# Optimization experiments

Hardware: AMD Instinct MI355X
Metric: run time of the kernel (lower is better)

## Reference

```python
import jax, jax.numpy as jnp
from jax import lax
import numpy as np

BATCH = 8
INPUT_LEN = 768
OUTPUT_LEN = 192
MULTISCALE = (1, 2, 4)
HIDDEN = 256          # HiPPO order N == spectral channels
MODES = 32            # min(32, min(output_len, input_len)//2)
NUM_FEAT = 64


def hippo_matrices(N, dt):
    """HiPPO-LegT continuous matrices, bilinear-discretized (scipy cont2discrete equiv)."""
    Q = np.arange(N, dtype=np.float64)
    R = (2 * Q + 1)[:, None]
    j, i = np.meshgrid(Q, Q)
    A = np.where(i < j, -1.0, (-1.0) ** (i - j + 1)) * R
    B = ((-1.0) ** Q[:, None]) * R  # [N,1]
    I = np.eye(N)
    ima = I - (dt / 2.0) * A
    Ad = np.linalg.solve(ima, I + (dt / 2.0) * A)
    Bd = np.linalg.solve(ima, B * dt).squeeze(-1)
    return Ad.astype(np.float32), Bd.astype(np.float32)


def legendre_eval_matrix(N, dt):
    """eval_matrix[t, n] = P_n(1 - 2*vals[t]), vals = arange(0,1,dt)."""
    vals = np.arange(0.0, 1.0, dt)
    x = 1.0 - 2.0 * vals
    P = np.zeros((N, len(vals)), dtype=np.float64)
    P[0] = 1.0
    if N > 1:
        P[1] = x
    for n in range(1, N - 1):
        P[n + 1] = ((2 * n + 1) * x * P[n] - n * P[n - 1]) / (n + 1)
    return P.T.astype(np.float32)  # [len(vals), N]


def setup_inputs() -> dict:
    key = jax.random.key(0)
    k1, k2, k3, k4 = jax.random.split(key, 4)
    scale = 1.0 / (HIDDEN * HIDDEN)
    return {
        "inputs": jax.random.normal(k1, (BATCH, INPUT_LEN, NUM_FEAT), jnp.float32),
        "spec_wr": scale * jax.random.uniform(k2, (3, HIDDEN, HIDDEN, MODES), jnp.float32),
        "spec_wi": scale * jax.random.uniform(k3, (3, HIDDEN, HIDDEN, MODES), jnp.float32),
        "mlp_w": 0.1 * jax.random.normal(k4, (1, 3), jnp.float32),
        "mlp_b": jnp.zeros((1,), jnp.float32),
    }


def _film_forward(inputs, spec_wr, spec_wi, mlp_w, mlp_b):
    B_, _, D = inputs.shape
    preds = []
    for idx, scale in enumerate(MULTISCALE):
        dt = 1.0 / OUTPUT_LEN / scale
        Ad_np, Bd_np = hippo_matrices(HIDDEN, dt)
        em_np = legendre_eval_matrix(HIDDEN, dt)[-OUTPUT_LEN:]  # [out_len, N]
        Ad = jnp.asarray(Ad_np)
        Bd = jnp.asarray(Bd_np)
        em = jnp.asarray(em_np)
        T = scale * OUTPUT_LEN
        # HiPPO recurrence: c_t = c_{t-1} @ A^T + f_t * B  (sequential scan over time)
        f = jnp.transpose(inputs[:, -T:], (1, 0, 2))  # [T, B, D]

        def step(c, f_t, Ad=Ad, Bd=Bd):
            c = c @ Ad.T + f_t[..., None] * Bd
            return c, c

        c0 = jnp.zeros((B_, D, HIDDEN), inputs.dtype)
        _, cs = lax.scan(step, c0, f)               # [T, B, D, N]
        x = jnp.transpose(cs, (1, 2, 3, 0))          # [B, D, N, T]
        # SpectralConv1d: rfft -> complex mixing on low modes -> irfft
        x_ft = jnp.fft.rfft(x)                       # [B, D, N, T//2+1]
        w = (spec_wr[idx] + 1j * spec_wi[idx]).astype(jnp.complex64)  # [N, N, modes]
        out_m = jnp.einsum('bjix,iox->bjox', x_ft[..., :MODES], w)    # [B, D, N, modes]
        nfreq = T // 2 + 1
        out_ft = jnp.concatenate(
            [out_m, jnp.zeros(out_m.shape[:-1] + (nfreq - MODES,), out_m.dtype)], axis=-1)
        x = jnp.fft.irfft(out_ft, n=T)               # [B, D, N, T]
        # input_len >= output_len -> pick time index output_len-1, then project with Legendre
        x_out = x[:, :, :, OUTPUT_LEN - 1]           # [B, D, N]
        preds.append(x_out @ em.T)                   # [B, D, out_len]
    pred = jnp.stack(preds, axis=-1)                 # [B, D, out_len, 3]
    pred = jnp.squeeze(pred @ mlp_w.T + mlp_b, -1)   # [B, D, out_len]
    return jnp.transpose(pred, (0, 2, 1))            # [B, out_len, D]


def reference(inputs, spec_wr, spec_wi, mlp_w, mlp_b):
    return _film_forward(inputs, spec_wr, spec_wi, mlp_w, mlp_b)
```

## Files before the change

### kernel.cpp

```cpp
#include <hip/hip_runtime.h>


#define OFF_MF64  0
#define OFF_YA    1572864
#define OFF_YB    3145728
#define OFF_Z     4718592
#define OFF_F     7864320
#define OFF_PIV   8650752
#define OFF_FLAG  8653824
#define OFF_AP0   10223616
#define OFF_AP1   11010048
#define OFF_BD    11796480
#define OFF_V     11800576
#define OFF_EM    14159872
#define OFF_P     14749696
#define OFF_K     16125952
#define OFF_U4    29298688
#define OFF_WT4   117440512
#define OFF_C32   167772160
#define OFF_SEG4  211812352

typedef _Float16 half8 __attribute__((ext_vector_type(8)));
typedef float f32x4 __attribute__((ext_vector_type(4)));

__device__ __forceinline__ double a_entry(int i, int j){
  double base = (i < j) ? -1.0 : (((i - j) & 1) ? 1.0 : -1.0);
  return base * (double)(2*i + 1);
}

__device__ __forceinline__ unsigned int dpp_umax(unsigned int x){
  unsigned int t;
  t = (unsigned int)__builtin_amdgcn_update_dpp((int)x, (int)x, 0x111, 0xF, 0xF, false); x = x > t ? x : t;
  t = (unsigned int)__builtin_amdgcn_update_dpp((int)x, (int)x, 0x112, 0xF, 0xF, false); x = x > t ? x : t;
  t = (unsigned int)__builtin_amdgcn_update_dpp((int)x, (int)x, 0x114, 0xF, 0xE, false); x = x > t ? x : t;
  t = (unsigned int)__builtin_amdgcn_update_dpp((int)x, (int)x, 0x118, 0xF, 0xC, false); x = x > t ? x : t;
  t = (unsigned int)__builtin_amdgcn_update_dpp((int)x, (int)x, 0x142, 0xA, 0xF, false); x = x > t ? x : t;
  t = (unsigned int)__builtin_amdgcn_update_dpp((int)x, (int)x, 0x143, 0xC, 0xF, false); x = x > t ? x : t;
  return x;
}

__global__ void k_init(double* __restrict__ Mf64, float* __restrict__ em,
                       int* __restrict__ flags){
  int s = blockIdx.y, i = blockIdx.x, j = threadIdx.x;
  if (i < 256){
    double dt = (1.0 / 192.0) / (double)(1 << s);
    double m = ((i == j) ? 1.0 : 0.0) - 0.5 * dt * a_entry(i, j);
    Mf64[((size_t)s*256 + i)*256 + j] = m;
  } else {
    if (j < 192){
      int T = 192 << s;
      double dt = (1.0 / 192.0) / (double)(1 << s);
      double x = 1.0 - 2.0 * ((double)(T - 192 + j) * dt);
      float* row = em + ((size_t)s*192 + j)*256;
      double p0 = 1.0, p1 = x;
      row[0] = 1.0f; row[1] = (float)x;
      for (int n = 1; n < 255; ++n){
        double p2 = ((double)(2*n+1) * x * p1 - (double)n * p0) / (double)(n+1);
        row[n+1] = (float)p2;
        p0 = p1; p1 = p2;
      }
    } else if (j < 200){
      flags[s*8 + (j - 192)] = 0;
    }
  }
}

__global__ __launch_bounds__(256) void k_gj(float* __restrict__ Fg,
                                            int* __restrict__ pivg,
                                            int* __restrict__ flags,
                                            double* __restrict__ Ya){
  int s = blockIdx.x >> 4;
  int g = blockIdx.x & 15;
  int r = threadIdx.x;
  int c0 = g*32;
  float row[32];
  if (g < 8){
    double dt = (1.0 / 192.0) / (double)(1 << s);
    #pragma unroll
    for (int j = 0; j < 32; ++j){
      int col = c0 + j;
      row[j] = (float)(((r == col) ? 1.0 : 0.0) - 0.5*dt*a_entry(r, col));
    }
  } else {
    #pragma unroll
    for (int j = 0; j < 32; ++j) row[j] = (r == c0 - 256 + j) ? 1.f : 0.f;
  }
  __shared__ float Fl[32*256];
  __shared__ float prow[2][32];
  __shared__ float prow1[32];
  __shared__ int pvs[32];
  __shared__ unsigned int wv[4];
  __shared__ int invp[256];
  int used = 0;
  int* flagS = flags + s*8;
  int nrep = (g < 8) ? g : 8;
  for (int kp = 0; kp < nrep; ++kp){
    if (r == 0){
      int cnt = 0;
      while (__hip_atomic_load(&flagS[kp], __ATOMIC_ACQUIRE, __HIP_MEMORY_SCOPE_AGENT) == 0){
        __builtin_amdgcn_s_sleep(8);
        if (++cnt > 100000000) break;
      }
    }
    __syncthreads();
    const float* Fp = Fg + ((size_t)(s*8 + kp))*8192;
    #pragma unroll
    for (int l = 0; l < 32; ++l) Fl[l*256 + r] = Fp[l*256 + r];
    if (r < 32) pvs[r] = pivg[s*256 + kp*32 + r];
    __syncthreads();
    #pragma unroll
    for (int l = 0; l < 32; ++l) if (pvs[l] == r) used = 1;
    for (int l = 0; l < 32; ++l){
      int piv = pvs[l];
      float fv = Fl[l*256 + r];
      if (r == piv){
        #pragma unroll
        for (int j = 0; j < 32; ++j){ row[j] *= fv; prow[l & 1][j] = row[j]; }
      }
      __syncthreads();
      if (r != piv){
        #pragma unroll
        for (int j = 0; j < 32; ++j) row[j] -= fv * prow[l & 1][j];
      }
    }
    __syncthreads();
  }
  if (g < 8){
    float freg[32];
    #pragma unroll
    for (int l = 0; l < 32; ++l){
      float av = fabsf(row[l]);
      unsigned int kb = __builtin_bit_cast(unsigned int, av);
      unsigned int key = used ? 0u : ((kb & 0xFFFFFF00u) | (unsigned int)(255 - r));
      key = dpp_umax(key);
      if ((r & 63) == 63) wv[r >> 6] = key;
      __syncthreads();
      unsigned int b0 = wv[0] > wv[1] ? wv[0] : wv[1];
      unsigned int b1 = wv[2] > wv[3] ? wv[2] : wv[3];
      unsigned int best = b0 > b1 ? b0 : b1;
      int piv = 255 - (int)(best & 0xFFu);
      if (r == piv){
        float inv = 1.0f / row[l];
        freg[l] = inv;
        used = 1;
        #pragma unroll
        for (int j = 0; j < 32; ++j){ row[j] *= inv; prow1[j] = row[j]; }
      }
      if (r == 0) pvs[l] = piv;
      __syncthreads();
      if (r != piv){
        float f = row[l];
        freg[l] = f;
        #pragma unroll
        for (int j = 0; j < 32; ++j) row[j] -= f * prow1[j];
      }
    }
    float* Fgp = Fg + ((size_t)(s*8 + g))*8192;
    #pragma unroll
    for (int l = 0; l < 32; ++l) Fgp[l*256 + r] = freg[l];
    if (r < 32) pivg[s*256 + g*32 + r] = pvs[r];
    __threadfence();
    __syncthreads();
    if (r == 0)
      __hip_atomic_store(&flagS[g], 1, __ATOMIC_RELEASE, __HIP_MEMORY_SCOPE_AGENT);
  } else {
    int p = pivg[s*256 + r];
    invp[p] = r;
    __syncthreads();
    int dst = invp[r];
    double* Yr = Ya + ((size_t)s*256 + dst)*256 + (c0 - 256);
    #pragma unroll
    for (int j = 0; j < 32; ++j) Yr[j] = (double)row[j];
  }
}

__global__ void k_mmZ(const double* __restrict__ M, const double* __restrict__ Y,
                      double* __restrict__ Z){
  int s = blockIdx.y;
  const double* A = M + (size_t)s*65536;
  const double* B = Y + (size_t)s*65536;
  int c = threadIdx.x, r0 = blockIdx.x * 8;
  double acc[8] = {0,0,0,0,0,0,0,0};
  for (int j = 0; j < 256; ++j){
    double b = B[(size_t)j*256 + c];
    #pragma unroll
    for (int q = 0; q < 8; ++q) acc[q] += A[(size_t)(r0+q)*256 + j] * b;
  }
  #pragma unroll
  for (int q = 0; q < 8; ++q) Z[(size_t)s*65536 + (size_t)(r0+q)*256 + c] = acc[q];
}

__global__ void k_mmN(const double* __restrict__ Y, const double* __restrict__ Z,
                      double* __restrict__ Yn){
  int s = blockIdx.y;
  const double* A = Y + (size_t)s*65536;
  const double* B = Z + (size_t)s*65536;
  int c = threadIdx.x, r0 = blockIdx.x * 8;
  double acc[8] = {0,0,0,0,0,0,0,0};
  for (int j = 0; j < 256; ++j){
    double b = B[(size_t)j*256 + c];
    #pragma unroll
    for (int q = 0; q < 8; ++q) acc[q] += A[(size_t)(r0+q)*256 + j] * b;
  }
  #pragma unroll
  for (int q = 0; q < 8; ++q)
    Yn[(size_t)s*65536 + (size_t)(r0+q)*256 + c] =
      2.0 * A[(size_t)(r0+q)*256 + c] - acc[q];
}

__global__ void k_final(const double* __restrict__ Y, float* __restrict__ Ad,
                        float* __restrict__ Bd, float* __restrict__ V){
  int s = blockIdx.y;
  const double* Ys = Y + (size_t)s*65536;
  if (blockIdx.x < 64){
    int c = threadIdx.x, r0 = blockIdx.x * 4;
    #pragma unroll
    for (int q = 0; q < 4; ++q){
      double v = 2.0 * Ys[(size_t)(r0+q)*256 + c] - ((r0+q) == c ? 1.0 : 0.0);
      Ad[(size_t)s*65536 + (size_t)(r0+q)*256 + c] = (float)v;
    }
  } else {
    int i = threadIdx.x;
    double dt = (1.0 / 192.0) / (double)(1 << s);
    double acc = 0.0;
    for (int j = 0; j < 256; ++j){
      double bj = dt * ((j & 1) ? -1.0 : 1.0) * (double)(2*j + 1);
      acc += Ys[(size_t)i*256 + j] * bj;
    }
    float b = (float)acc;
    Bd[s*256 + i] = b;
    V[((size_t)s*768 + 0)*256 + i] = b;
  }
}

__global__ void k_level(const float* __restrict__ Pin, float* __restrict__ Pout,
                        float* __restrict__ V, int L, int noSquare){
  int s = blockIdx.y;
  const float* A = Pin + (size_t)s*65536;
  int bx = blockIdx.x;
  if (bx < 64){
    if (noSquare) return;
    int c = threadIdx.x, r0 = bx * 4;
    float acc[4] = {0,0,0,0};
    for (int k = 0; k < 256; ++k){
      float b = A[(size_t)k*256 + c];
      #pragma unroll
      for (int q = 0; q < 4; ++q) acc[q] += A[(size_t)(r0+q)*256 + k] * b;
    }
    #pragma unroll
    for (int q = 0; q < 4; ++q) Pout[(size_t)s*65536 + (size_t)(r0+q)*256 + c] = acc[q];
  } else {
    int j = threadIdx.x;
    if (j >= L || L + j >= 768) return;
    int r0 = (bx - 64) * 4;
    float* Vs = V + (size_t)s*768*256;
    float acc[4] = {0,0,0,0};
    for (int k = 0; k < 256; ++k){
      float v = Vs[(size_t)j*256 + k];
      #pragma unroll
      for (int q = 0; q < 4; ++q) acc[q] += A[(size_t)(r0+q)*256 + k] * v;
    }
    #pragma unroll
    for (int q = 0; q < 4; ++q) Vs[(size_t)(L+j)*256 + r0 + q] = acc[q];
  }
}

__global__ void k_wt(const float* __restrict__ wr, const float* __restrict__ wi,
                     float* __restrict__ Wt4){
  int s = blockIdx.x, i = blockIdx.y, tid = threadIdx.x;
  size_t srcbase = ((size_t)s*256 + i)*256;
  float* dst = Wt4 + ((size_t)s*256 + i)*16384;
  for (int ph = 0; ph < 64; ++ph){
    int col = ph*256 + tid;
    int kl = col >> 9, ri = (col >> 8) & 1, o = col & 255;
    const float* src = ri ? wi : wr;
    dst[col] = src[(srcbase + o)*32 + kl];
  }
}

__device__ __forceinline__ void splitf16(float x, unsigned short &h, unsigned short &l){
  _Float16 hf = (_Float16)x;
  _Float16 lf = (_Float16)(x - (float)hf);
  h = __builtin_bit_cast(unsigned short, hf);
  l = __builtin_bit_cast(unsigned short, lf);
}
__device__ __forceinline__ unsigned int pk(unsigned short a, unsigned short b){
  return (unsigned int)a | ((unsigned int)b << 16);
}

__global__ __launch_bounds__(256) void k_ugemm(const float* __restrict__ V,
                                               const float* __restrict__ Wt4,
                                               float* __restrict__ U){
  int s = blockIdx.z;
  int Ts = 192 << s;
  int mt = blockIdx.y;
  if (mt*64 >= Ts) return;
  int nb = blockIdx.x * 64;
  const float* Vs = V + (size_t)s*768*256;
  const float* Bm = Wt4 + (size_t)s*256*16384;
  __shared__ unsigned int Ah[4*65*4], Al[4*65*4];
  __shared__ unsigned int Bh[4*65*4], Bl[4*65*4];
  int tid = threadIdx.x;
  int lane = tid & 63;
  int w = tid >> 6;
  int m0 = (w >> 1) * 32, n0 = (w & 1) * 32;
  int ml = lane & 15, quad = lane >> 4;
  f32x4 acc[2][2];
  #pragma unroll
  for (int t = 0; t < 2; ++t)
    #pragma unroll
    for (int u = 0; u < 2; ++u) acc[t][u] = (f32x4){0.f,0.f,0.f,0.f};

  int am = tid >> 2, akf = tid & 3;
  int bn = tid & 63, bq = tid >> 6;

  for (int kk = 0; kk < 8; ++kk){
    if (kk) __syncthreads();
    {
      const float* ap = &Vs[(size_t)(mt*64 + am)*256 + kk*32 + akf*8];
      float4 a0 = *(const float4*)ap;
      float4 a1 = *(const float4*)(ap + 4);
      unsigned short h[8], l[8];
      splitf16(a0.x*16.f, h[0], l[0]); splitf16(a0.y*16.f, h[1], l[1]);
      splitf16(a0.z*16.f, h[2], l[2]); splitf16(a0.w*16.f, h[3], l[3]);
      splitf16(a1.x*16.f, h[4], l[4]); splitf16(a1.y*16.f, h[5], l[5]);
      splitf16(a1.z*16.f, h[6], l[6]); splitf16(a1.w*16.f, h[7], l[7]);
      int base = (akf*65 + am)*4;
      *(uint4*)&Ah[base] = make_uint4(pk(h[0],h[1]), pk(h[2],h[3]), pk(h[4],h[5]), pk(h[6],h[7]));
      *(uint4*)&Al[base] = make_uint4(pk(l[0],l[1]), pk(l[2],l[3]), pk(l[4],l[5]), pk(l[6],l[7]));
    }
    {
      unsigned short h[8], l[8];
      #pragma unroll
      for (int j = 0; j < 8; ++j){
        float b = Bm[(size_t)(kk*32 + bq*8 + j)*16384 + nb + bn];
        splitf16(b*65536.f, h[j], l[j]);
      }
      int base = (bq*65 + bn)*4;
      *(uint4*)&Bh[base] = make_uint4(pk(h[0],h[1]), pk(h[2],h[3]), pk(h[4],h[5]), pk(h[6],h[7]));
      *(uint4*)&Bl[base] = make_uint4(pk(l[0],l[1]), pk(l[2],l[3]), pk(l[4],l[5]), pk(l[6],l[7]));
    }
    __syncthreads();
    half8 ah[2], al[2], bh[2], bl[2];
    #pragma unroll
    for (int t = 0; t < 2; ++t){
      int idx = (quad*65 + m0 + 16*t + ml)*4;
      ah[t] = *(const half8*)&Ah[idx];
      al[t] = *(const half8*)&Al[idx];
    }
    #pragma unroll
    for (int u = 0; u < 2; ++u){
      int idx = (quad*65 + n0 + 16*u + ml)*4;
      bh[u] = *(const half8*)&Bh[idx];
      bl[u] = *(const half8*)&Bl[idx];
    }
    #pragma unroll
    for (int t = 0; t < 2; ++t)
      #pragma unroll
      for (int u = 0; u < 2; ++u){
        acc[t][u] = __builtin_amdgcn_mfma_f32_16x16x32_f16(ah[t], bh[u], acc[t][u], 0, 0, 0);
        acc[t][u] = __builtin_amdgcn_mfma_f32_16x16x32_f16(ah[t], bl[u], acc[t][u], 0, 0, 0);
        acc[t][u] = __builtin_amdgcn_mfma_f32_16x16x32_f16(al[t], bh[u], acc[t][u], 0, 0, 0);
      }
  }
  int ub = (s == 0) ? 0 : (s == 1 ? 192 : 576);
  const float unscale = 1.0f / 1048576.0f;
  #pragma unroll
  for (int t = 0; t < 2; ++t)
    #pragma unroll
    for (int u = 0; u < 2; ++u){
      int row = ub + mt*64 + m0 + 16*t + quad*4;
      int col = nb + n0 + 16*u + ml;
      #pragma unroll
      for (int r = 0; r < 4; ++r)
        U[(size_t)(row + r)*16384 + col] = acc[t][u][r] * unscale;
    }
}

__global__ void k_scanA(float* __restrict__ U, float* __restrict__ Seg){
  int seg = blockIdx.x;
  int kl  = blockIdx.y;
  int s   = blockIdx.z;
  int k = kl;
  int T = 192 << s;
  int Ls = T >> 3;
  int m0 = seg * Ls;
  int ub = (s == 0) ? 0 : (s == 1 ? 192 : 576);
  int o = threadIdx.x;
  float* Ur = U + ((size_t)(ub + m0))*16384 + kl*512 + o;
  float th = 6.283185307179586f / (float)T;
  int im = (k * m0) % T;
  float Zr = 0.f, Zi = 0.f;
  #pragma unroll 4
  for (int i = 0; i < Ls; ++i){
    float ur = Ur[0];
    float ui = Ur[256];
    float sa, ca; __sincosf(th * (float)im, &sa, &ca);
    Zr += ca*ur + sa*ui;
    Zi += ca*ui - sa*ur;
    Ur[0] = Zr; Ur[256] = Zi;
    im += k; if (im >= T) im -= T;
    Ur += 16384;
  }
  float* Sg = Seg + (((size_t)(s*32 + kl)*8 + seg)*2)*256 + o;
  Sg[0] = Zr; Sg[256] = Zi;
}

__global__ void k_scanC(const float* __restrict__ U, const float* __restrict__ Seg,
                        float* __restrict__ C32){
  int seg = blockIdx.x, kl = blockIdx.y, s = blockIdx.z;
  int k = kl;
  int T = 192 << s;
  int Ls = T >> 3;
  int m0 = seg * Ls;
  int ub = (s == 0) ? 0 : (s == 1 ? 192 : 576);
  int o = threadIdx.x;
  float offr = 0.f, offi = 0.f;
  const float* Sg = Seg + ((size_t)(s*32 + kl)*8)*512 + o;
  for (int j = 0; j < seg; ++j){ offr += Sg[(size_t)j*512]; offi += Sg[(size_t)j*512 + 256]; }
  const float* Ur = U + ((size_t)(ub + m0))*16384 + kl*512 + o;
  float* Cb = C32 + ((size_t)kl*1344 + ub)*256 + o;
  float ckT = ((k == 0) ? 1.0f : 2.0f) / (float)T;
  float th = 6.283185307179586f / (float)T;
  int ib = (k * (192 + m0)) % T;
  #pragma unroll 4
  for (int i = 0; i < Ls; ++i){
    int m = m0 + i;
    float zr = offr + Ur[0];
    float zi = offi + Ur[256];
    float sb, cb; __sincosf(th * (float)ib, &sb, &cb);
    Cb[(size_t)(T-1-m)*256] = ckT * (zr*cb - zi*sb);
    ib += k; if (ib >= T) ib -= T;
    Ur += 16384;
  }
}

__global__ void k_reduce(const float* __restrict__ C32, float* __restrict__ P){
  int row = blockIdx.x;
  int o = threadIdx.x;
  float a = 0.f;
  #pragma unroll
  for (int kl = 0; kl < 32; ++kl) a += C32[((size_t)kl*1344 + row)*256 + o];
  P[(size_t)row*256 + o] = a;
}

__global__ __launch_bounds__(256) void k_K(const float* __restrict__ em,
                                           const float* __restrict__ P,
                                           const float* __restrict__ mlpw,
                                           float* __restrict__ K){
  int tn = blockIdx.x;
  int tmb = blockIdx.y;
  __shared__ float Es[16][68];
  __shared__ float Ps[16][68];
  int tid = threadIdx.x;
  int tm = tid >> 4, tnn = tid & 15;
  int srow = tid >> 2;
  int acol4 = (tid & 3) * 4;
  float acc[4][4];
  #pragma unroll
  for (int a = 0; a < 4; ++a)
    #pragma unroll
    for (int b = 0; b < 4; ++b) acc[a][b] = 0.f;
  for (int s = 0; s < 3; ++s){
    int T = 192 << s;
    int off = 768 - T;
    if (tn*64 < off) continue;
    int ub = (s == 0) ? 0 : (s == 1 ? 192 : 576);
    float mw = mlpw[s];
    const float* ems = em + ((size_t)s*192 + tmb*64)*256;
    const float* Pb = P + ((size_t)ub + (tn*64 - off))*256;
    float sacc[4][4];
    #pragma unroll
    for (int a = 0; a < 4; ++a)
      #pragma unroll
      for (int b = 0; b < 4; ++b) sacc[a][b] = 0.f;
    for (int k0 = 0; k0 < 256; k0 += 16){
      float4 e4 = *(const float4*)&ems[(size_t)srow*256 + k0 + acol4];
      Es[acol4+0][srow] = e4.x; Es[acol4+1][srow] = e4.y;
      Es[acol4+2][srow] = e4.z; Es[acol4+3][srow] = e4.w;
      float4 p4 = *(const float4*)&Pb[(size_t)srow*256 + k0 + acol4];
      Ps[acol4+0][srow] = p4.x; Ps[acol4+1][srow] = p4.y;
      Ps[acol4+2][srow] = p4.z; Ps[acol4+3][srow] = p4.w;
      __syncthreads();
      #pragma unroll
      for (int k = 0; k < 16; ++k){
        float av[4], bv[4];
        *(float4*)av = *(const float4*)&Es[k][tm*4];
        *(float4*)bv = *(const float4*)&Ps[k][tnn*4];
        #pragma unroll
        for (int a = 0; a < 4; ++a)
          #pragma unroll
          for (int b = 0; b < 4; ++b) sacc[a][b] += av[a]*bv[b];
      }
      __syncthreads();
    }
    #pragma unroll
    for (int a = 0; a < 4; ++a)
      #pragma unroll
      for (int b = 0; b < 4; ++b) acc[a][b] += mw * sacc[a][b];
  }
  int to0 = tmb*64 + tm*4;
  int tg0 = tn*64 + tnn*4;
  #pragma unroll
  for (int a = 0; a < 4; ++a){
    float4 o4 = make_float4(acc[a][0], acc[a][1], acc[a][2], acc[a][3]);
    *(float4*)&K[(size_t)(to0+a)*768 + tg0] = o4;
  }
}

__global__ __launch_bounds__(256) void k_out(const float* __restrict__ K,
                                             const float* __restrict__ inp,
                                             const float* __restrict__ mlpb,
                                             float* __restrict__ out){
  int to = blockIdx.x, b = blockIdx.y;
  int d = threadIdx.x & 63;
  int w = threadIdx.x >> 6;
  const float* Kr = K + (size_t)to*768 + w*192;
  const float* ip = inp + (size_t)b*768*64 + (size_t)(w*192)*64 + d;
  float acc = 0.f;
  #pragma unroll 4
  for (int i = 0; i < 192; ++i) acc += Kr[i] * ip[(size_t)i*64];
  __shared__ float red[4][64];
  red[w][d] = acc;
  __syncthreads();
  if (w == 0)
    out[((size_t)b*192 + to)*64 + d] =
      red[0][d] + red[1][d] + red[2][d] + red[3][d] + mlpb[0];
}

extern "C" void kernel_launch(void* const* d_in, const int* in_sizes, int n_in,
                              void* d_out, int out_size, void* d_ws, size_t ws_size,
                              hipStream_t stream){
  const float* inputs  = (const float*)d_in[0];
  const float* spec_wr = (const float*)d_in[1];
  const float* spec_wi = (const float*)d_in[2];
  const float* mlp_w   = (const float*)d_in[3];
  const float* mlp_b   = (const float*)d_in[4];
  float* out = (float*)d_out;
  char* ws = (char*)d_ws;

  double* Mf64 = (double*)(ws + OFF_MF64);
  double* Ya   = (double*)(ws + OFF_YA);
  double* Yb   = (double*)(ws + OFF_YB);
  double* Zb   = (double*)(ws + OFF_Z);
  float* Fg   = (float*)(ws + OFF_F);
  int*   pivg = (int*)(ws + OFF_PIV);
  int*   flags= (int*)(ws + OFF_FLAG);
  float* AP0  = (float*)(ws + OFF_AP0);
  float* AP1  = (float*)(ws + OFF_AP1);
  float* Bd   = (float*)(ws + OFF_BD);
  float* V    = (float*)(ws + OFF_V);
  float* em   = (float*)(ws + OFF_EM);
  float* P    = (float*)(ws + OFF_P);
  float* Km   = (float*)(ws + OFF_K);
  float* U4   = (float*)(ws + OFF_U4);
  float* Wt4  = (float*)(ws + OFF_WT4);
  float* C32  = (float*)(ws + OFF_C32);
  float* Seg4 = (float*)(ws + OFF_SEG4);

  k_init<<<dim3(257,3), 256, 0, stream>>>(Mf64, em, flags);
  k_gj<<<48, 256, 0, stream>>>(Fg, pivg, flags, Ya);
  for (int it = 0; it < 2; ++it){
    double* yi = (it & 1) ? Yb : Ya;
    double* yo = (it & 1) ? Ya : Yb;
    k_mmZ<<<dim3(32,3), 256, 0, stream>>>(Mf64, yi, Zb);
    k_mmN<<<dim3(32,3), 256, 0, stream>>>(yi, Zb, yo);
  }
  k_final<<<dim3(65,3), 256, 0, stream>>>(Ya, AP0, Bd, V);

  float* pin = AP0; float* pout = AP1;
  for (int L = 1; L <= 512; L <<= 1){
    k_level<<<dim3(128,3), 256, 0, stream>>>(pin, pout, V, L, (L == 512) ? 1 : 0);
    float* t = pin; pin = pout; pout = t;
  }

  k_wt<<<dim3(3,256), 256, 0, stream>>>(spec_wr, spec_wi, Wt4);
  k_ugemm<<<dim3(256,12,3), 256, 0, stream>>>(V, Wt4, U4);
  k_scanA<<<dim3(8,32,3), 256, 0, stream>>>(U4, Seg4);
  k_scanC<<<dim3(8,32,3), 256, 0, stream>>>(U4, Seg4, C32);
  k_reduce<<<1344, 256, 0, stream>>>(C32, P);
  k_K<<<dim3(12,3), 256, 0, stream>>>(em, P, mlp_w, Km);
  k_out<<<dim3(192,8), 256, 0, stream>>>(Km, inputs, mlp_b, out);
}
```

Measured before the change: 823.0 us.

## Apply prior Gauss-Jordan panels as block rank-32 updates instead of sequential eliminations

```diff
diff --git a/kernel.cpp b/kernel.cpp
--- a/kernel.cpp
+++ b/kernel.cpp
@@ -65,7 +65,7 @@
   }
 }
 
-__global__ __launch_bounds__(256) void k_gj(float* __restrict__ Fg,
+__global__ __launch_bounds__(256) void k_gj(float* __restrict__ Cg,
                                             int* __restrict__ pivg,
                                             int* __restrict__ flags,
                                             double* __restrict__ Ya){
@@ -73,63 +73,83 @@
   int g = blockIdx.x & 15;
   int r = threadIdx.x;
   int c0 = g*32;
-  float row[32];
+  float trow[32];
   if (g < 8){
     double dt = (1.0 / 192.0) / (double)(1 << s);
     #pragma unroll
     for (int j = 0; j < 32; ++j){
       int col = c0 + j;
-      row[j] = (float)(((r == col) ? 1.0 : 0.0) - 0.5*dt*a_entry(r, col));
+      trow[j] = (float)(((r == col) ? 1.0 : 0.0) - 0.5*dt*a_entry(r, col));
     }
   } else {
     #pragma unroll
-    for (int j = 0; j < 32; ++j) row[j] = (r == c0 - 256 + j) ? 1.f : 0.f;
-  }
-  __shared__ float Fl[32*256];
-  __shared__ float prow[2][32];
-  __shared__ float prow1[32];
+    for (int j = 0; j < 32; ++j) trow[j] = (r == c0 - 256 + j) ? 1.f : 0.f;
+  }
+  __shared__ float yl[32][32];
   __shared__ int pvs[32];
+  __shared__ int pivAll[256];
+  __shared__ float prow1[64];
   __shared__ unsigned int wv[4];
   __shared__ int invp[256];
   int used = 0;
   int* flagS = flags + s*8;
   int nrep = (g < 8) ? g : 8;
+
   for (int kp = 0; kp < nrep; ++kp){
     if (r == 0){
       int cnt = 0;
       while (__hip_atomic_load(&flagS[kp], __ATOMIC_ACQUIRE, __HIP_MEMORY_SCOPE_AGENT) == 0){
-        __builtin_amdgcn_s_sleep(8);
+        __builtin_amdgcn_s_sleep(2);
         if (++cnt > 100000000) break;
       }
     }
     __syncthreads();
-    const float* Fp = Fg + ((size_t)(s*8 + kp))*8192;
-    #pragma unroll
-    for (int l = 0; l < 32; ++l) Fl[l*256 + r] = Fp[l*256 + r];
-    if (r < 32) pvs[r] = pivg[s*256 + kp*32 + r];
+    if (r < 32){
+      int p = pivg[s*256 + kp*32 + r];
+      pvs[r] = p;
+      if (g >= 8) pivAll[kp*32 + r] = p;
+    }
+    float cp[32];
+    const float* Cr = Cg + ((size_t)(s*8 + kp))*8192 + r*32;
+    #pragma unroll
+    for (int l = 0; l < 32; l += 4){
+      float4 v = *(const float4*)&Cr[l];
+      cp[l] = v.x; cp[l+1] = v.y; cp[l+2] = v.z; cp[l+3] = v.w;
+    }
     __syncthreads();
-    #pragma unroll
-    for (int l = 0; l < 32; ++l) if (pvs[l] == r) used = 1;
+    if (g < 8){
+      #pragma unroll
+      for (int l = 0; l < 32; ++l) if (pvs[l] == r) used = 1;
+    }
+    #pragma unroll
     for (int l = 0; l < 32; ++l){
-      int piv = pvs[l];
-      float fv = Fl[l*256 + r];
-      if (r == piv){
+      if (pvs[l] == r){
         #pragma unroll
-        for (int j = 0; j < 32; ++j){ row[j] *= fv; prow[l & 1][j] = row[j]; }
-      }
-      __syncthreads();
-      if (r != piv){
-        #pragma unroll
-        for (int j = 0; j < 32; ++j) row[j] -= fv * prow[l & 1][j];
+        for (int j = 0; j < 32; ++j) yl[l][j] = trow[j];
       }
     }
     __syncthreads();
-  }
+    #pragma unroll
+    for (int l = 0; l < 32; ++l){
+      float y[32];
+      #pragma unroll
+      for (int j = 0; j < 32; j += 4){
+        float4 v = *(const float4*)&yl[l][j];
+        y[j] = v.x; y[j+1] = v.y; y[j+2] = v.z; y[j+3] = v.w;
+      }
+      float c = cp[l];
+      #pragma unroll
+      for (int j = 0; j < 32; ++j) trow[j] += c * y[j];
+    }
+  }
+
   if (g < 8){
-    float freg[32];
+    float xrow[32];
+    #pragma unroll
+    for (int l = 0; l < 32; ++l) xrow[l] = 0.f;
     #pragma unroll
     for (int l = 0; l < 32; ++l){
-      float av = fabsf(row[l]);
+      float av = fabsf(trow[l]);
       unsigned int kb = __builtin_bit_cast(unsigned int, av);
       unsigned int key = used ? 0u : ((kb & 0xFFFFFF00u) | (unsigned int)(255 - r));
       key = dpp_umax(key);
@@ -140,37 +160,40 @@
       unsigned int best = b0 > b1 ? b0 : b1;
       int piv = 255 - (int)(best & 0xFFu);
       if (r == piv){
-        float inv = 1.0f / row[l];
-        freg[l] = inv;
+        float inv = 1.0f / trow[l];
         used = 1;
+        xrow[l] = 1.0f;
         #pragma unroll
-        for (int j = 0; j < 32; ++j){ row[j] *= inv; prow1[j] = row[j]; }
+        for (int j = 0; j < 32; ++j){ trow[j] *= inv; prow1[j] = trow[j]; }
+        #pragma unroll
+        for (int m = 0; m < 32; ++m){ xrow[m] *= inv; prow1[32 + m] = xrow[m]; }
       }
       if (r == 0) pvs[l] = piv;
       __syncthreads();
       if (r != piv){
-        float f = row[l];
-        freg[l] = f;
+        float f = trow[l];
         #pragma unroll
-        for (int j = 0; j < 32; ++j) row[j] -= f * prow1[j];
-      }
-    }
-    float* Fgp = Fg + ((size_t)(s*8 + g))*8192;
-    #pragma unroll
-    for (int l = 0; l < 32; ++l) Fgp[l*256 + r] = freg[l];
+        for (int j = 0; j < 32; ++j) trow[j] -= f * prow1[j];
+        #pragma unroll
+        for (int m = 0; m < 32; ++m) xrow[m] -= f * prow1[32 + m];
+      }
+    }
+    float* Cw = Cg + ((size_t)(s*8 + g))*8192 + r*32;
+    #pragma unroll
+    for (int l = 0; l < 32; ++l)
+      Cw[l] = xrow[l] - ((pvs[l] == r) ? 1.0f : 0.0f);
     if (r < 32) pivg[s*256 + g*32 + r] = pvs[r];
     __threadfence();
     __syncthreads();
     if (r == 0)
       __hip_atomic_store(&flagS[g], 1, __ATOMIC_RELEASE, __HIP_MEMORY_SCOPE_AGENT);
   } else {
-    int p = pivg[s*256 + r];
-    invp[p] = r;
+    invp[pivAll[r]] = r;
     __syncthreads();
     int dst = invp[r];
     double* Yr = Ya + ((size_t)s*256 + dst)*256 + (c0 - 256);
     #pragma unroll
-    for (int j = 0; j < 32; ++j) Yr[j] = (double)row[j];
+    for (int j = 0; j < 32; ++j) Yr[j] = (double)trow[j];
   }
 }
 
@@ -543,7 +566,7 @@
   double* Ya   = (double*)(ws + OFF_YA);
   double* Yb   = (double*)(ws + OFF_YB);
   double* Zb   = (double*)(ws + OFF_Z);
-  float* Fg   = (float*)(ws + OFF_F);
+  float* Cg   = (float*)(ws + OFF_F);
   int*   pivg = (int*)(ws + OFF_PIV);
   int*   flags= (int*)(ws + OFF_FLAG);
   float* AP0  = (float*)(ws + OFF_AP0);
@@ -559,7 +582,7 @@
   float* Seg4 = (float*)(ws + OFF_SEG4);
 
   k_init<<<dim3(257,3), 256, 0, stream>>>(Mf64, em, flags);
-  k_gj<<<48, 256, 0, stream>>>(Fg, pivg, flags, Ya);
+  k_gj<<<48, 256, 0, stream>>>(Cg, pivg, flags, Ya);
   for (int it = 0; it < 2; ++it){
     double* yi = (it & 1) ? Yb : Ya;
     double* yo = (it & 1) ? Ya : Yb;
```

Result: slower. 860.0 us (+4.5%).
